# Kernel tuning notes

Hardware: AMD Instinct MI355X
Metric: run time of the kernel (lower is better)

The kernel has to match this reference:

```python
import jax, jax.numpy as jnp
import numpy as np

B, T, E = 4, 2048, 1024
H, HS = 16, 64

def setup_inputs() -> dict:
    key = jax.random.key(0)
    ks = jax.random.split(key, 6)
    return {
        "x": jax.random.normal(ks[0], (B, T, E), dtype=jnp.float32),
        "Wq": jax.random.normal(ks[1], (H, E, HS), dtype=jnp.float32) * 0.02,
        "Wk": jax.random.normal(ks[2], (H, E, HS), dtype=jnp.float32) * 0.02,
        "Wv": jax.random.normal(ks[3], (H, E, HS), dtype=jnp.float32) * 0.02,
        "proj_w": jax.random.normal(ks[4], (E, H * HS), dtype=jnp.float32) * 0.02,
        "proj_b": jax.random.normal(ks[5], (E,), dtype=jnp.float32) * 0.02,
    }

def reference(x, Wq, Wk, Wv, proj_w, proj_b):
    b, t, e = x.shape
    h, _, hs = Wq.shape
    # NOTE: original uses .view() (raw reshape, not transpose) from [b,t,h,hs]
    # to [h,b,t,hs]; we replicate that exactly for faithfulness.
    q = jnp.einsum('bxy,iyk->bxik', x, Wq).reshape(h, b, t, hs)
    k = jnp.einsum('bxy,iyk->bxik', x, Wk).reshape(h, b, t, hs)
    v = jnp.einsum('bxy,iyk->bxik', x, Wv).reshape(h, b, t, hs)
    # scores: [h, b, t, t], scaled by 1/sqrt(head_size)
    wei = jnp.einsum('hbqd,hbkd->hbqk', q, k) * (hs ** -0.5)
    causal = jnp.tril(jnp.ones((t, t), dtype=bool))  # [t, t]
    wei = jnp.where(causal, wei, -jnp.inf)
    wei = jax.nn.softmax(wei, axis=-1)  # dropout is identity in eval
    out = jnp.einsum('hbqk,hbkd->hbqd', wei, v)
    # raw reshape [h,b,t,hs] -> [b,t,h*hs], matching torch .view()
    out = out.reshape(b, t, h * hs)
    out = out @ proj_w.T + proj_b  # nn.Linear
    return out
```

## Files before the change

kernel.cpp:

```cpp
#include <hip/hip_runtime.h>

typedef unsigned short u16;
typedef __attribute__((ext_vector_type(8))) __bf16 bf16x8;
typedef __attribute__((ext_vector_type(8))) short short8;
typedef __attribute__((ext_vector_type(4))) float f32x4;
typedef __attribute__((ext_vector_type(4))) unsigned short ushort4v;

__device__ __forceinline__ u16 f2bf(float f) {
  unsigned u = __builtin_bit_cast(unsigned, f);
  u += 0x7fffu + ((u >> 16) & 1u);
  return (u16)(u >> 16);
}

__device__ __forceinline__ float exp2_hw(float x) {
  float r; asm("v_exp_f32 %0, %1" : "=v"(r) : "v"(x)); return r;
}
__device__ __forceinline__ unsigned cvt_pk_bf16(float a, float b) {
  unsigned r; asm("v_cvt_pk_bf16_f32 %0, %1, %2" : "=v"(r) : "v"(a), "v"(b)); return r;
}

__device__ __forceinline__ void gload_lds16(const void* g, void* l) {
  __builtin_amdgcn_global_load_lds(
      (__attribute__((address_space(1))) void*)g,
      (__attribute__((address_space(3))) void*)l, 16, 0, 0);
}

__device__ __forceinline__ void BAR() {
  asm volatile("" ::: "memory");
  __builtin_amdgcn_s_barrier();
  asm volatile("" ::: "memory");
}

#define MFMA16(a, b, c) __builtin_amdgcn_mfma_f32_16x16x32_bf16(a, b, c, 0, 0, 0)

#define QSCALE 0.1803368801111204f


__global__ __launch_bounds__(256)
void prep_kernel(const float* __restrict__ x, const float* __restrict__ Wq,
                 const float* __restrict__ Wk, const float* __restrict__ Wv,
                 const float* __restrict__ pw, u16* __restrict__ Xb,
                 u16* __restrict__ Wcat, u16* __restrict__ PWt) {
  const int b = blockIdx.x, tid = threadIdx.x;
  if (b < 8192) {
    int i = b * 256 + tid;
    float4 v = ((const float4*)x)[i];
    union { u16 u[4]; uint2 v2; } r;
    r.u[0] = f2bf(v.x); r.u[1] = f2bf(v.y); r.u[2] = f2bf(v.z); r.u[3] = f2bf(v.w);
    ((uint2*)Xb)[i] = r.v2;
  } else if (b < 8960) {
    __shared__ u16 lds[64 * 68];
    int bb = b - 8192;
    int sel = bb >> 8, rem = bb & 255;
    int h = rem >> 4, e0 = (rem & 15) * 64;
    const float* W = (sel == 0) ? Wq : (sel == 1) ? Wk : Wv;
    const float* src = W + ((size_t)h * 1024 + e0) * 64;
#pragma unroll
    for (int i = 0; i < 4; i++) {
      int idx = i * 1024 + tid * 4;
      int e = idx >> 6, hs = idx & 63;
      float4 v = *(const float4*)&src[idx];
      u16* d = &lds[e * 68 + hs];
      d[0] = f2bf(v.x); d[1] = f2bf(v.y); d[2] = f2bf(v.z); d[3] = f2bf(v.w);
    }
    __syncthreads();
#pragma unroll
    for (int i = 0; i < 2; i++) {
      int u = i * 256 + tid;
      int hs = u >> 3, ec = u & 7;
      union { u16 q[8]; uint4 v; } ou;
#pragma unroll
      for (int e = 0; e < 8; e++) ou.q[e] = lds[(ec * 8 + e) * 68 + hs];
      size_t n = (size_t)sel * 1024 + h * 64 + hs;
      *(uint4*)&Wcat[n * 1024 + e0 + ec * 8] = ou.v;
    }
  } else {
    int i = (b - 8960) * 256 + tid;
    float4 v = ((const float4*)pw)[i];
    union { u16 u[4]; uint2 v2; } r;
    r.u[0] = f2bf(v.x); r.u[1] = f2bf(v.y); r.u[2] = f2bf(v.z); r.u[3] = f2bf(v.w);
    ((uint2*)PWt)[i] = r.v2;
  }
}


template<int OUT_BF16>
__global__ __launch_bounds__(512, 2)
void gemm3b(const u16* __restrict__ A, const u16* __restrict__ BT,
            void* __restrict__ Cout, const float* __restrict__ bias,
            int M, int N, int K, int gy, int qcols) {
  __shared__ u16 a_lds[3][128 * 64];
  __shared__ u16 b_lds[3][256 * 64];
  const int nwg = gridDim.x;
  const int qch = nwg >> 3;
  const int wg = (blockIdx.x & 7) * qch + (blockIdx.x >> 3);
  const int bx = wg / gy, by = wg % gy;
  const int tid = threadIdx.x;
  const int lane = tid & 63;
  const int w = tid >> 6;
  const int wr = w >> 2, wc = w & 3;
  const int mBase = by * 128, nBase = bx * 256;
  const int l15 = lane & 15, l4 = lane >> 4;
  const int nkt = K >> 6;

  f32x4 acc[4][4] = {};

  auto STAGE_A = [&](int s, int kt) {
#pragma unroll
    for (int j = 0; j < 2; j++) {
      int e = j * 4096 + tid * 8;
      int row = e >> 6;
      int c = ((e >> 3) & 7) ^ (row & 7);
      gload_lds16(A + (size_t)(mBase + row) * K + kt * 64 + c * 8, &a_lds[s][e]);
    }
  };
  auto STAGE_B = [&](int s, int kt) {
#pragma unroll
    for (int j = 0; j < 4; j++) {
      int e = j * 4096 + tid * 8;
      int row = e >> 6;
      int c = ((e >> 3) & 7) ^ (row & 7);
      gload_lds16(BT + (size_t)(nBase + row) * K + kt * 64 + c * 8, &b_lds[s][e]);
    }
  };

  STAGE_A(0, 0); STAGE_B(0, 0);
  STAGE_A(1, 1); STAGE_B(1, 1);
  asm volatile("s_waitcnt vmcnt(6)" ::: "memory");
  BAR();

  int s0 = 0, s1 = 1, s2 = 2;
  for (int t = 0; t < nkt; t++) {
    const int t2 = (t + 2 < nkt) ? t + 2 : t + 2 - nkt;
    bf16x8 AF[4][2], BF[2][2];

#pragma unroll
    for (int m = 0; m < 4; m++) {
      int row = wr * 64 + m * 16 + l15;
#pragma unroll
      for (int ks = 0; ks < 2; ks++) {
        int ch = (ks * 4 + l4) ^ (row & 7);
        AF[m][ks] = *(const bf16x8*)&a_lds[s0][row * 64 + ch * 8];
      }
    }
#pragma unroll
    for (int n = 0; n < 2; n++) {
      int row = wc * 64 + n * 16 + l15;
#pragma unroll
      for (int ks = 0; ks < 2; ks++) {
        int ch = (ks * 4 + l4) ^ (row & 7);
        BF[n][ks] = *(const bf16x8*)&b_lds[s0][row * 64 + ch * 8];
      }
    }
    STAGE_A(s2, t2);
    STAGE_B(s2, t2);
    __builtin_amdgcn_s_setprio(1);
#pragma unroll
    for (int m = 0; m < 4; m++)
#pragma unroll
      for (int n = 0; n < 2; n++) {
        acc[m][n] = MFMA16(AF[m][0], BF[n][0], acc[m][n]);
        acc[m][n] = MFMA16(AF[m][1], BF[n][1], acc[m][n]);
      }
    __builtin_amdgcn_s_setprio(0);

#pragma unroll
    for (int n = 0; n < 2; n++) {
      int row = wc * 64 + 32 + n * 16 + l15;
#pragma unroll
      for (int ks = 0; ks < 2; ks++) {
        int ch = (ks * 4 + l4) ^ (row & 7);
        BF[n][ks] = *(const bf16x8*)&b_lds[s0][row * 64 + ch * 8];
      }
    }
    __builtin_amdgcn_s_setprio(1);
#pragma unroll
    for (int m = 0; m < 4; m++)
#pragma unroll
      for (int n = 0; n < 2; n++) {
        acc[m][2 + n] = MFMA16(AF[m][0], BF[n][0], acc[m][2 + n]);
        acc[m][2 + n] = MFMA16(AF[m][1], BF[n][1], acc[m][2 + n]);
      }
    __builtin_amdgcn_s_setprio(0);

    asm volatile("s_waitcnt vmcnt(6)" ::: "memory");
    BAR();
    int tmp = s0; s0 = s1; s1 = s2; s2 = tmp;
  }

#pragma unroll
  for (int mi = 0; mi < 4; mi++) {
    int row = mBase + wr * 64 + mi * 16 + l4 * 4;
#pragma unroll
    for (int ni = 0; ni < 4; ni++) {
      int col = nBase + wc * 64 + ni * 16 + l15;
      float scl = (col < qcols) ? QSCALE : 1.f;
#pragma unroll
      for (int j = 0; j < 4; j++) {
        float v = acc[mi][ni][j];
        if (OUT_BF16) {
          ((u16*)Cout)[(size_t)(row + j) * N + col] = f2bf(v * scl);
        } else {
          ((float*)Cout)[(size_t)(row + j) * N + col] = v + bias[col];
        }
      }
    }
  }
}


__global__ __launch_bounds__(256)
void vt_build(const u16* __restrict__ qkv, u16* __restrict__ vt) {
  __shared__ u16 lds[64 * 66];
  const int hb = blockIdx.x >> 5, tc = blockIdx.x & 31;
  const int t0 = tc * 64, tid = threadIdx.x;
#pragma unroll
  for (int i = 0; i < 2; i++) {
    int idx = i * 2048 + tid * 8;
    int tl = idx >> 6, d0 = idx & 63;
    int r = hb * 2048 + t0 + tl;
    const u16* src = &qkv[(size_t)(r >> 4) * 3072 + 2048 + (r & 15) * 64 + d0];
    uint4 v = *(const uint4*)src;
    u16* dst = &lds[tl * 66 + d0];
    *(unsigned*)(dst + 0) = v.x; *(unsigned*)(dst + 2) = v.y;
    *(unsigned*)(dst + 4) = v.z; *(unsigned*)(dst + 6) = v.w;
  }
  __syncthreads();
#pragma unroll
  for (int i = 0; i < 2; i++) {
    int idx = i * 2048 + tid * 8;
    int d = idx >> 6, tl0 = idx & 63;
    union { u16 u[8]; uint4 v; } ou;
#pragma unroll
    for (int e = 0; e < 8; e++) ou.u[e] = lds[(tl0 + e) * 66 + d];
    *(uint4*)&vt[(size_t)hb * 131072 + (size_t)d * 2048 + t0 + tl0] = ou.v;
  }
}


__global__ __launch_bounds__(512, 2)
void attn_kernel(const u16* __restrict__ qkv, const u16* __restrict__ vtg,
                 u16* __restrict__ att) {
  __shared__ u16 k_lds[2][64 * 64];
  __shared__ u16 v_lds[2][64 * 64];
  __shared__ u16 p_lds[8][32 * 72];

  const int xcd = blockIdx.x & 7;
  const int c = blockIdx.x >> 3;
  const int hb = xcd * 8 + (c & 7);
  const int qb = 7 - (c >> 3);
  const int tid = threadIdx.x;
  const int lane = tid & 63, w = tid >> 6;
  const int l15 = lane & 15, l4 = lane >> 4;
  const int qbase = qb * 256 + w * 32;
  const int nkt = 4 * qb + 4;

  bf16x8 aQ[2][2];
#pragma unroll
  for (int qs = 0; qs < 2; qs++) {
    int t = qbase + qs * 16 + l15;
    int r = hb * 2048 + t;
    size_t base = (size_t)(r >> 4) * 3072 + (r & 15) * 64;
#pragma unroll
    for (int kc = 0; kc < 2; kc++)
      aQ[qs][kc] = *(const bf16x8*)&qkv[base + kc * 32 + l4 * 8];
  }

  f32x4 o[2][4] = {};
  float lp[2] = {0.f, 0.f};

  auto STAGE = [&](int buf, int kt) {
    {
      int U = tid * 8;
      int row = U >> 6;
      int chunk = ((U >> 3) & 7) ^ (row & 7);
      int rK = hb * 2048 + kt * 64 + row;
      gload_lds16(&qkv[(size_t)(rK >> 4) * 3072 + 1024 + (rK & 15) * 64 + chunk * 8],
                  &k_lds[buf][U]);
    }
    {
      int U = tid * 8;
      int row = U >> 6;
      int chunk = ((U >> 3) & 7) ^ (row & 7);
      gload_lds16(&vtg[(size_t)hb * 131072 + (size_t)row * 2048 + kt * 64 + chunk * 8],
                  &v_lds[buf][U]);
    }
  };

  STAGE(0, 0);
  asm volatile("s_waitcnt vmcnt(0)" ::: "memory");
  BAR();

  for (int kt = 0; kt < nkt; kt++) {
    if (kt + 1 < nkt) STAGE((kt + 1) & 1, kt + 1);
    const int cur = kt & 1;
    const bool active = (kt * 64 <= qbase + 31);
    if (active) {
      f32x4 st[4][2];
      __builtin_amdgcn_s_setprio(1);
#pragma unroll
      for (int n = 0; n < 4; n++) {
        int row = n * 16 + l15;
        int sw = (row & 7) << 3;
        bf16x8 kf0 = *(const bf16x8*)&k_lds[cur][row * 64 + ((0 + l4 * 8) ^ sw)];
        bf16x8 kf1 = *(const bf16x8*)&k_lds[cur][row * 64 + ((32 + l4 * 8) ^ sw)];
#pragma unroll
        for (int qs = 0; qs < 2; qs++) {
          f32x4 a = {0.f, 0.f, 0.f, 0.f};
          a = MFMA16(kf0, aQ[qs][0], a);
          a = MFMA16(kf1, aQ[qs][1], a);
          st[n][qs] = a;
        }
      }
      __builtin_amdgcn_s_setprio(0);
      const bool full = (kt * 64 + 63 <= qbase);
#pragma unroll
      for (int qs = 0; qs < 2; qs++) {
        int q = qbase + qs * 16 + l15;
#pragma unroll
        for (int n = 0; n < 4; n++) {
          float p[4];
#pragma unroll
          for (int j = 0; j < 4; j++) {
            float v = st[n][qs][j];
            if (!full) {
              int k = kt * 64 + n * 16 + l4 * 4 + j;
              v = (k > q) ? -INFINITY : v;
            }
            p[j] = exp2_hw(v);
            lp[qs] += p[j];
          }
          uint2 pk;
          pk.x = cvt_pk_bf16(p[0], p[1]);
          pk.y = cvt_pk_bf16(p[2], p[3]);
          *(uint2*)&p_lds[w][(qs * 16 + l15) * 72 + n * 16 + l4 * 4] = pk;
        }
      }
#pragma unroll
      for (int ks = 0; ks < 2; ks++) {
        bf16x8 pf[2];
#pragma unroll
        for (int qs = 0; qs < 2; qs++)
          pf[qs] = *(const bf16x8*)&p_lds[w][(qs * 16 + l15) * 72 + ks * 32 + l4 * 8];
        __builtin_amdgcn_s_setprio(1);
#pragma unroll
        for (int nd = 0; nd < 4; nd++) {
          int row = nd * 16 + l15;
          int sw = (row & 7) << 3;
          bf16x8 vf = *(const bf16x8*)&v_lds[cur][row * 64 + ((ks * 32 + l4 * 8) ^ sw)];
#pragma unroll
          for (int qs = 0; qs < 2; qs++)
            o[qs][nd] = MFMA16(vf, pf[qs], o[qs][nd]);
        }
        __builtin_amdgcn_s_setprio(0);
      }
    }
    asm volatile("s_waitcnt vmcnt(0)" ::: "memory");
    BAR();
  }

#pragma unroll
  for (int qs = 0; qs < 2; qs++) {
    float l = lp[qs];
    l += __shfl_xor(l, 16);
    l += __shfl_xor(l, 32);
    float rl = 1.f / l;
    int q = qbase + qs * 16 + l15;
    size_t rbase = ((size_t)hb * 2048 + q) * 64;
#pragma unroll
    for (int nd = 0; nd < 4; nd++) {
      ushort4v ov;
#pragma unroll
      for (int j = 0; j < 4; j++) ov[j] = f2bf(o[qs][nd][j] * rl);
      *(ushort4v*)&att[rbase + nd * 16 + l4 * 4] = ov;
    }
  }
}


extern "C" void kernel_launch(void* const* d_in, const int* in_sizes, int n_in,
                              void* d_out, int out_size, void* d_ws, size_t ws_size,
                              hipStream_t stream) {
  const float* x  = (const float*)d_in[0];
  const float* Wq = (const float*)d_in[1];
  const float* Wk = (const float*)d_in[2];
  const float* Wv = (const float*)d_in[3];
  const float* pw = (const float*)d_in[4];
  const float* pb = (const float*)d_in[5];
  float* out = (float*)d_out;

  char* ws = (char*)d_ws;
  u16* Xb   = (u16*)(ws);
  u16* VTg  = (u16*)(ws);
  u16* Wcat = (u16*)(ws + (16u << 20));
  u16* PWt  = (u16*)(ws + (22u << 20));
  u16* QKV  = (u16*)(ws + (24u << 20));
  u16* ATT  = (u16*)(ws + (72u << 20));

  prep_kernel<<<9984, 256, 0, stream>>>(x, Wq, Wk, Wv, pw, Xb, Wcat, PWt);

  gemm3b<1><<<768, 512, 0, stream>>>(Xb, Wcat, QKV, nullptr, 8192, 3072, 1024, 64, 1024);

  vt_build<<<2048, 256, 0, stream>>>(QKV, VTg);

  attn_kernel<<<512, 512, 0, stream>>>(QKV, VTg, ATT);

  gemm3b<0><<<256, 512, 0, stream>>>(ATT, PWt, out, pb, 8192, 1024, 1024, 64, 0);
}
```

Measured before the change: 195.3 us.

## Switch attention to 32x32 MFMA and pass P through registers via permlane swap

Rewrites the attention inner loop to use 32x32x16 bf16 MFMA tiles instead of 16x16x32. The softmax probabilities are repacked in registers with permlane32_swap rather than round-tripped through a per-wave LDS buffer, so p_lds is removed. This cuts LDS traffic and shrinks shared memory, and the launch bound is raised to 4 blocks per CU to exploit that. The higher occupancy target may force register spills given the 32-float accumulators.

```diff
diff --git a/kernel.cpp b/kernel.cpp
--- a/kernel.cpp
+++ b/kernel.cpp
@@ -2,9 +2,10 @@
 
 typedef unsigned short u16;
 typedef __attribute__((ext_vector_type(8))) __bf16 bf16x8;
-typedef __attribute__((ext_vector_type(8))) short short8;
 typedef __attribute__((ext_vector_type(4))) float f32x4;
+typedef __attribute__((ext_vector_type(16))) float f32x16;
 typedef __attribute__((ext_vector_type(4))) unsigned short ushort4v;
+typedef __attribute__((ext_vector_type(2))) unsigned uint2v;
 
 __device__ __forceinline__ u16 f2bf(float f) {
   unsigned u = __builtin_bit_cast(unsigned, f);
@@ -32,6 +33,7 @@
 }
 
 #define MFMA16(a, b, c) __builtin_amdgcn_mfma_f32_16x16x32_bf16(a, b, c, 0, 0, 0)
+#define MFMA32(a, b, c) __builtin_amdgcn_mfma_f32_32x32x16_bf16(a, b, c, 0, 0, 0)
 
 #define QSCALE 0.1803368801111204f
 
@@ -238,12 +240,11 @@
 }
 
 
-__global__ __launch_bounds__(512, 2)
+__global__ __launch_bounds__(512, 4)
 void attn_kernel(const u16* __restrict__ qkv, const u16* __restrict__ vtg,
                  u16* __restrict__ att) {
   __shared__ u16 k_lds[2][64 * 64];
   __shared__ u16 v_lds[2][64 * 64];
-  __shared__ u16 p_lds[8][32 * 72];
 
   const int xcd = blockIdx.x & 7;
   const int c = blockIdx.x >> 3;
@@ -251,23 +252,22 @@
   const int qb = 7 - (c >> 3);
   const int tid = threadIdx.x;
   const int lane = tid & 63, w = tid >> 6;
-  const int l15 = lane & 15, l4 = lane >> 4;
+  const int l31 = lane & 31, l5 = lane >> 5;
   const int qbase = qb * 256 + w * 32;
   const int nkt = 4 * qb + 4;
 
-  bf16x8 aQ[2][2];
-#pragma unroll
-  for (int qs = 0; qs < 2; qs++) {
-    int t = qbase + qs * 16 + l15;
+  bf16x8 qf[4];
+  {
+    int t = qbase + l31;
     int r = hb * 2048 + t;
     size_t base = (size_t)(r >> 4) * 3072 + (r & 15) * 64;
 #pragma unroll
-    for (int kc = 0; kc < 2; kc++)
-      aQ[qs][kc] = *(const bf16x8*)&qkv[base + kc * 32 + l4 * 8];
-  }
-
-  f32x4 o[2][4] = {};
-  float lp[2] = {0.f, 0.f};
+    for (int d = 0; d < 4; d++)
+      qf[d] = *(const bf16x8*)&qkv[base + d * 16 + l5 * 8];
+  }
+
+  f32x16 o0 = {}, o1 = {};
+  float lp = 0.f;
 
   auto STAGE = [&](int buf, int kt) {
     {
@@ -296,83 +296,75 @@
     const int cur = kt & 1;
     const bool active = (kt * 64 <= qbase + 31);
     if (active) {
-      f32x4 st[4][2];
-      __builtin_amdgcn_s_setprio(1);
-#pragma unroll
-      for (int n = 0; n < 4; n++) {
-        int row = n * 16 + l15;
-        int sw = (row & 7) << 3;
-        bf16x8 kf0 = *(const bf16x8*)&k_lds[cur][row * 64 + ((0 + l4 * 8) ^ sw)];
-        bf16x8 kf1 = *(const bf16x8*)&k_lds[cur][row * 64 + ((32 + l4 * 8) ^ sw)];
-#pragma unroll
-        for (int qs = 0; qs < 2; qs++) {
-          f32x4 a = {0.f, 0.f, 0.f, 0.f};
-          a = MFMA16(kf0, aQ[qs][0], a);
-          a = MFMA16(kf1, aQ[qs][1], a);
-          st[n][qs] = a;
-        }
-      }
-      __builtin_amdgcn_s_setprio(0);
       const bool full = (kt * 64 + 63 <= qbase);
-#pragma unroll
-      for (int qs = 0; qs < 2; qs++) {
-        int q = qbase + qs * 16 + l15;
-#pragma unroll
-        for (int n = 0; n < 4; n++) {
-          float p[4];
-#pragma unroll
-          for (int j = 0; j < 4; j++) {
-            float v = st[n][qs][j];
-            if (!full) {
-              int k = kt * 64 + n * 16 + l4 * 4 + j;
-              v = (k > q) ? -INFINITY : v;
-            }
-            p[j] = exp2_hw(v);
-            lp[qs] += p[j];
-          }
-          uint2 pk;
-          pk.x = cvt_pk_bf16(p[0], p[1]);
-          pk.y = cvt_pk_bf16(p[2], p[3]);
-          *(uint2*)&p_lds[w][(qs * 16 + l15) * 72 + n * 16 + l4 * 4] = pk;
-        }
-      }
-#pragma unroll
-      for (int ks = 0; ks < 2; ks++) {
-        bf16x8 pf[2];
-#pragma unroll
-        for (int qs = 0; qs < 2; qs++)
-          pf[qs] = *(const bf16x8*)&p_lds[w][(qs * 16 + l15) * 72 + ks * 32 + l4 * 8];
+      const int q = qbase + l31;
+#pragma unroll
+      for (int kb = 0; kb < 2; kb++) {
+        int krow = kb * 32 + l31;
+        int ksw = krow & 7;
+        f32x16 st = {};
         __builtin_amdgcn_s_setprio(1);
 #pragma unroll
-        for (int nd = 0; nd < 4; nd++) {
-          int row = nd * 16 + l15;
-          int sw = (row & 7) << 3;
-          bf16x8 vf = *(const bf16x8*)&v_lds[cur][row * 64 + ((ks * 32 + l4 * 8) ^ sw)];
-#pragma unroll
-          for (int qs = 0; qs < 2; qs++)
-            o[qs][nd] = MFMA16(vf, pf[qs], o[qs][nd]);
+        for (int t = 0; t < 4; t++) {
+          bf16x8 kf = *(const bf16x8*)&k_lds[cur][krow * 64 + ((t * 2 + l5) ^ ksw) * 8];
+          st = MFMA32(kf, qf[t], st);
         }
         __builtin_amdgcn_s_setprio(0);
+        float p[16];
+#pragma unroll
+        for (int r = 0; r < 16; r++) {
+          float v = st[r];
+          if (!full) {
+            int k = kt * 64 + kb * 32 + (r & 3) + 8 * (r >> 2) + 4 * l5;
+            v = (k > q) ? -INFINITY : v;
+          }
+          p[r] = exp2_hw(v);
+          lp += p[r];
+        }
+#pragma unroll
+        for (int kc = 0; kc < 2; kc++) {
+          unsigned w0 = cvt_pk_bf16(p[kc * 8 + 0], p[kc * 8 + 1]);
+          unsigned w1 = cvt_pk_bf16(p[kc * 8 + 2], p[kc * 8 + 3]);
+          unsigned w2 = cvt_pk_bf16(p[kc * 8 + 4], p[kc * 8 + 5]);
+          unsigned w3 = cvt_pk_bf16(p[kc * 8 + 6], p[kc * 8 + 7]);
+          uint2v s0 = __builtin_amdgcn_permlane32_swap(w0, w2, false, false);
+          uint2v s1 = __builtin_amdgcn_permlane32_swap(w1, w3, false, false);
+          union { unsigned u[4]; bf16x8 v; } pf;
+          pf.u[0] = s0.x; pf.u[1] = s1.x; pf.u[2] = s0.y; pf.u[3] = s1.y;
+          __builtin_amdgcn_s_setprio(1);
+          {
+            int row0 = l31;
+            int ch0 = (kb * 4 + kc * 2 + l5) ^ (row0 & 7);
+            bf16x8 vf0 = *(const bf16x8*)&v_lds[cur][row0 * 64 + ch0 * 8];
+            o0 = MFMA32(vf0, pf.v, o0);
+            int row1 = 32 + l31;
+            int ch1 = (kb * 4 + kc * 2 + l5) ^ (row1 & 7);
+            bf16x8 vf1 = *(const bf16x8*)&v_lds[cur][row1 * 64 + ch1 * 8];
+            o1 = MFMA32(vf1, pf.v, o1);
+          }
+          __builtin_amdgcn_s_setprio(0);
+        }
       }
     }
     asm volatile("s_waitcnt vmcnt(0)" ::: "memory");
     BAR();
   }
 
-#pragma unroll
-  for (int qs = 0; qs < 2; qs++) {
-    float l = lp[qs];
-    l += __shfl_xor(l, 16);
-    l += __shfl_xor(l, 32);
-    float rl = 1.f / l;
-    int q = qbase + qs * 16 + l15;
+  lp += __shfl_xor(lp, 32);
+  float rl = 1.f / lp;
+  {
+    int q = qbase + l31;
     size_t rbase = ((size_t)hb * 2048 + q) * 64;
 #pragma unroll
-    for (int nd = 0; nd < 4; nd++) {
-      ushort4v ov;
-#pragma unroll
-      for (int j = 0; j < 4; j++) ov[j] = f2bf(o[qs][nd][j] * rl);
-      *(ushort4v*)&att[rbase + nd * 16 + l4 * 4] = ov;
+    for (int g = 0; g < 4; g++) {
+      uint2 wv;
+      wv.x = cvt_pk_bf16(o0[4 * g + 0] * rl, o0[4 * g + 1] * rl);
+      wv.y = cvt_pk_bf16(o0[4 * g + 2] * rl, o0[4 * g + 3] * rl);
+      *(uint2*)&att[rbase + g * 8 + 4 * l5] = wv;
+      uint2 wu;
+      wu.x = cvt_pk_bf16(o1[4 * g + 0] * rl, o1[4 * g + 1] * rl);
+      wu.y = cvt_pk_bf16(o1[4 * g + 2] * rl, o1[4 * g + 3] * rl);
+      *(uint2*)&att[rbase + 32 + g * 8 + 4 * l5] = wu;
     }
   }
 }
```

Result: faster. 186.7 us (-4.4%).
